# Performance work log

Hardware: AMD Instinct MI355X
Metric: run time of the kernel (lower is better)

## Reference

```python
import jax, jax.numpy as jnp
import numpy as np


def setup_inputs() -> dict:
    key = jax.random.key(0)
    k1, k2 = jax.random.split(key)
    outputs = jax.random.normal(k1, (8192, 64), dtype=jnp.float32)
    labels = jax.random.randint(k2, (8192,), 0, 10)
    return {"outputs": outputs, "labels": labels}


def reference(outputs, labels):
    # outputs: [b, d], labels: [b]
    # Original: distances[i, j] = sqrt(||o_i - o_j||_2) * (-1 if labels differ else 5)
    # for j > i, then summed. sqrt(norm) == (sum of squared diffs) ** 0.25.
    b = outputs.shape[0]
    sq = jnp.sum(outputs * outputs, axis=1)                      # [b]
    gram = outputs @ outputs.T                                   # [b, b]
    d2 = jnp.maximum(sq[:, None] + sq[None, :] - 2.0 * gram, 0.0)  # squared L2 dists
    upper = jnp.triu(jnp.ones((b, b), dtype=bool), k=1)          # j > i mask
    factor = jnp.where(labels[:, None] != labels[None, :], -1.0, 5.0)
    d2_safe = jnp.where(upper, d2, 1.0)                          # avoid 0**0.25 grad issues
    dist = d2_safe ** 0.25                                       # sqrt(L2 norm)
    return jnp.sum(jnp.where(upper, dist * factor, 0.0))
```

## Files before the change

### kernel.cpp

```cpp
#include <hip/hip_runtime.h>


typedef __bf16 bf16x8 __attribute__((ext_vector_type(8)));
typedef float  f32x4  __attribute__((ext_vector_type(4)));
typedef int    i32x4  __attribute__((ext_vector_type(4)));

#define BT    128
#define DK    64
#define PANEL (128 * DK)

__device__ __forceinline__ float qroot(float x) {
    return __builtin_amdgcn_sqrtf(__builtin_amdgcn_sqrtf(x));
}
__device__ __forceinline__ unsigned short rne_bf16(float v) {
    const unsigned u = __builtin_bit_cast(unsigned, v);
    return (unsigned short)((u + 0x7fffu + ((u >> 16) & 1u)) >> 16);
}

__global__ __launch_bounds__(256)
void ss_prep(const float* __restrict__ O, unsigned short* __restrict__ Obf,
             float* __restrict__ sqb) {
    const int row  = blockIdx.x * 4 + (threadIdx.x >> 6);
    const int lane = threadIdx.x & 63;
    const float v = O[(size_t)row * 64 + lane];
    const unsigned short w = rne_bf16(v);
    Obf[(size_t)row * 64 + lane] = w;
    const float wf = __builtin_bit_cast(float, (unsigned)w << 16);
    float s = wf * wf;
    #pragma unroll
    for (int off = 32; off; off >>= 1) s += __shfl_xor(s, off);
    if (lane == 0) sqb[row] = s;
}

__global__ __launch_bounds__(256, 4)
void ss_mfma(const unsigned short* __restrict__ Obf, const float* __restrict__ sqb,
             const int* __restrict__ L, float* __restrict__ partials, int nt) {
    const int t = blockIdx.x;
    const float fnt = (float)nt + 0.5f;
    int ti = (int)floorf(fnt - sqrtf(fnt * fnt - 2.0f * (float)t));
    if (ti < 0) ti = 0;
    if (ti > nt - 1) ti = nt - 1;
    while (ti > 0 && ti * nt - (ti * (ti - 1)) / 2 > t) --ti;
    while ((ti + 1) * nt - ((ti + 1) * ti) / 2 <= t) ++ti;
    const int tj = ti + (t - (ti * nt - (ti * (ti - 1)) / 2));

    const int tid  = threadIdx.x;
    const int wave = tid >> 6, lane = tid & 63;
    const int wr = wave >> 1, wc = wave & 1;
    const bool diag = (ti == tj);

    __shared__ unsigned short lds[2 * PANEL];

    {
        const unsigned short* srcA = Obf + (size_t)(ti * BT) * DK;
        const unsigned short* srcB = Obf + (size_t)(tj * BT) * DK;
        bf16x8 ra[4], rb[4];
        #pragma unroll
        for (int k = 0; k < 4; ++k) {
            const int id = k * 256 + tid;
            ra[k] = *(const bf16x8*)(srcA + id * 8);
            rb[k] = *(const bf16x8*)(srcB + id * 8);
        }
        #pragma unroll
        for (int k = 0; k < 4; ++k) {
            const int id   = k * 256 + tid;
            const int row  = id >> 3, c = id & 7;
            const int slot = (c ^ (row & 7)) * 8;
            *(bf16x8*)(&lds[row * DK + slot])         = ra[k];
            *(bf16x8*)(&lds[PANEL + row * DK + slot]) = rb[k];
        }
    }
    __syncthreads();

    const int lrow = lane & 15;
    const int kq   = lane >> 4;
    const int r0   = ti * BT + wr * 64;
    const int x0   = (kq       ^ (lrow & 7)) * 8;
    const int x1   = ((kq + 4) ^ (lrow & 7)) * 8;

    float accs = 0.0f;

    if (!(diag && (wc < wr))) {
        f32x4 sqi[4]; i32x4 li[4];
        #pragma unroll
        for (int f = 0; f < 4; ++f) {
            const int ib = r0 + f * 16 + (kq << 2);
            sqi[f] = *(const f32x4*)(sqb + ib);
            li[f]  = *(const i32x4*)(L + ib);
        }
        const bool masked = diag && (wr == wc);

        bf16x8 afr[4][2];
        #pragma unroll
        for (int i = 0; i < 4; ++i) {
            const int rbase = (wr * 64 + i * 16 + lrow) * DK;
            afr[i][0] = *(const bf16x8*)(&lds[rbase + x0]);
            afr[i][1] = *(const bf16x8*)(&lds[rbase + x1]);
        }

        #pragma unroll
        for (int jh = 0; jh < 2; ++jh) {
            bf16x8 bfr[2][2];
            #pragma unroll
            for (int g = 0; g < 2; ++g) {
                const int rbase = PANEL + (wc * 64 + jh * 32 + g * 16 + lrow) * DK;
                bfr[g][0] = *(const bf16x8*)(&lds[rbase + x0]);
                bfr[g][1] = *(const bf16x8*)(&lds[rbase + x1]);
            }

            f32x4 acc[4][2];
            #pragma unroll
            for (int i = 0; i < 4; ++i)
                #pragma unroll
                for (int g = 0; g < 2; ++g)
                    acc[i][g] = (f32x4){0.f, 0.f, 0.f, 0.f};

            #pragma unroll
            for (int i = 0; i < 4; ++i)
                #pragma unroll
                for (int g = 0; g < 2; ++g) {
                    acc[i][g] = __builtin_amdgcn_mfma_f32_16x16x32_bf16(afr[i][0], bfr[g][0], acc[i][g], 0, 0, 0);
                    acc[i][g] = __builtin_amdgcn_mfma_f32_16x16x32_bf16(afr[i][1], bfr[g][1], acc[i][g], 0, 0, 0);
                }

            const int c0 = tj * BT + wc * 64 + jh * 32;
            #pragma unroll
            for (int g = 0; g < 2; ++g) {
                const int j    = c0 + g * 16 + lrow;
                const float sj = sqb[j];
                const int  ljv = L[j];
                if (masked) {
                    #pragma unroll
                    for (int fi = 0; fi < 4; ++fi) {
                        const int ib = r0 + fi * 16 + (kq << 2);
                        #pragma unroll
                        for (int r = 0; r < 4; ++r) {
                            float d2 = fmaf(-2.0f, acc[fi][g][r], sqi[fi][r] + sj);
                            d2 = fmaxf(d2, 0.0f);
                            const float dist = qroot(d2);
                            const float fac  = (li[fi][r] != ljv) ? -1.0f : 5.0f;
                            accs += (j > ib + r) ? dist * fac : 0.0f;
                        }
                    }
                } else {
                    #pragma unroll
                    for (int fi = 0; fi < 4; ++fi) {
                        #pragma unroll
                        for (int r = 0; r < 4; ++r) {
                            float d2 = fmaf(-2.0f, acc[fi][g][r], sqi[fi][r] + sj);
                            d2 = fmaxf(d2, 0.0f);
                            const float dist = qroot(d2);
                            const float fac  = (li[fi][r] != ljv) ? -1.0f : 5.0f;
                            accs = fmaf(dist, fac, accs);
                        }
                    }
                }
            }
        }
    }

    #pragma unroll
    for (int off = 32; off > 0; off >>= 1) accs += __shfl_down(accs, off);
    __syncthreads();
    float* fsc = (float*)lds;
    if (lane == 0) fsc[wave] = accs;
    __syncthreads();
    if (tid == 0) partials[t] = (fsc[0] + fsc[1]) + (fsc[2] + fsc[3]);
}

__global__ void ss_reduce_kernel(const float* __restrict__ partials, int n,
                                 float* __restrict__ out) {
    __shared__ float s[4];
    const int tid = threadIdx.x;
    float acc = 0.0f;
    for (int idx = tid; idx < n; idx += 256) acc += partials[idx];
    #pragma unroll
    for (int off = 32; off > 0; off >>= 1) acc += __shfl_down(acc, off);
    if ((tid & 63) == 0) s[tid >> 6] = acc;
    __syncthreads();
    if (tid == 0) out[0] = (s[0] + s[1]) + (s[2] + s[3]);
}

extern "C" void kernel_launch(void* const* d_in, const int* in_sizes, int n_in,
                              void* d_out, int out_size, void* d_ws, size_t ws_size,
                              hipStream_t stream) {
    const float* O = (const float*)d_in[0];
    const int*   L = (const int*)d_in[1];
    float* out = (float*)d_out;

    const int b    = in_sizes[1];
    const int nt   = b / BT;
    const int ntri = nt * (nt + 1) / 2;

    char* ws = (char*)d_ws;
    float*          partials = (float*)ws;
    float*          sqb      = (float*)(ws + (64 << 10));
    unsigned short* Obf      = (unsigned short*)(ws + (128 << 10));

    ss_prep<<<b / 4, 256, 0, stream>>>(O, Obf, sqb);
    ss_mfma<<<ntri, 256, 0, stream>>>(Obf, sqb, L, partials, nt);
    ss_reduce_kernel<<<1, 256, 0, stream>>>(partials, ntri, out);
}
```

Baseline: 30.36 us.

## Switch to per-wave 64x64 triangle tiles with wave-private LDS and no block sync

Each wave now owns one 64x64 upper-triangular tile pair and stages its own A/B panels into a private LDS slice, replacing the 128x128 block tile shared by four waves. Barriers and the LDS cross-wave reduction go away, and diagonal-tile waste drops because sub-tiles below the diagonal are no longer launched idle. The cost is more global loads per output element, since panels are reused across fewer outputs, and more partials to reduce. With nt=128 the triangle count is 8256, which is even, so ntri/2 blocks cover every tile.

```diff
diff --git a/kernel.cpp b/kernel.cpp
--- a/kernel.cpp
+++ b/kernel.cpp
@@ -5,9 +5,9 @@
 typedef float  f32x4  __attribute__((ext_vector_type(4)));
 typedef int    i32x4  __attribute__((ext_vector_type(4)));
 
-#define BT    128
-#define DK    64
-#define PANEL (128 * DK)
+#define WT     64
+#define DK     64
+#define WPANEL (WT * DK)
 
 __device__ __forceinline__ float qroot(float x) {
     return __builtin_amdgcn_sqrtf(__builtin_amdgcn_sqrtf(x));
@@ -32,10 +32,13 @@
     if (lane == 0) sqb[row] = s;
 }
 
-__global__ __launch_bounds__(256, 4)
+__global__ __launch_bounds__(128, 2)
 void ss_mfma(const unsigned short* __restrict__ Obf, const float* __restrict__ sqb,
              const int* __restrict__ L, float* __restrict__ partials, int nt) {
-    const int t = blockIdx.x;
+    const int tid  = threadIdx.x;
+    const int wave = tid >> 6, lane = tid & 63;
+    const int t    = blockIdx.x * 2 + wave;
+
     const float fnt = (float)nt + 0.5f;
     int ti = (int)floorf(fnt - sqrtf(fnt * fnt - 2.0f * (float)t));
     if (ti < 0) ti = 0;
@@ -43,116 +46,111 @@
     while (ti > 0 && ti * nt - (ti * (ti - 1)) / 2 > t) --ti;
     while ((ti + 1) * nt - ((ti + 1) * ti) / 2 <= t) ++ti;
     const int tj = ti + (t - (ti * nt - (ti * (ti - 1)) / 2));
-
-    const int tid  = threadIdx.x;
-    const int wave = tid >> 6, lane = tid & 63;
-    const int wr = wave >> 1, wc = wave & 1;
     const bool diag = (ti == tj);
 
-    __shared__ unsigned short lds[2 * PANEL];
+    const int lrow = lane & 15;
+    const int kq   = lane >> 4;
+    const int r0   = ti * WT;
+
+    __shared__ unsigned short lds[2 * 2 * WPANEL];
+    unsigned short* ldsA = &lds[wave * 2 * WPANEL];
+    unsigned short* ldsB = ldsA + WPANEL;
 
     {
-        const unsigned short* srcA = Obf + (size_t)(ti * BT) * DK;
-        const unsigned short* srcB = Obf + (size_t)(tj * BT) * DK;
-        bf16x8 ra[4], rb[4];
+        const unsigned short* srcA = Obf + (size_t)(ti * WT) * DK;
+        const unsigned short* srcB = Obf + (size_t)(tj * WT) * DK;
+        bf16x8 ra[8], rb[8];
         #pragma unroll
-        for (int k = 0; k < 4; ++k) {
-            const int id = k * 256 + tid;
+        for (int k = 0; k < 8; ++k) {
+            const int id = k * 64 + lane;
             ra[k] = *(const bf16x8*)(srcA + id * 8);
             rb[k] = *(const bf16x8*)(srcB + id * 8);
         }
         #pragma unroll
-        for (int k = 0; k < 4; ++k) {
-            const int id   = k * 256 + tid;
+        for (int k = 0; k < 8; ++k) {
+            const int id   = k * 64 + lane;
             const int row  = id >> 3, c = id & 7;
             const int slot = (c ^ (row & 7)) * 8;
-            *(bf16x8*)(&lds[row * DK + slot])         = ra[k];
-            *(bf16x8*)(&lds[PANEL + row * DK + slot]) = rb[k];
+            *(bf16x8*)(&ldsA[row * DK + slot]) = ra[k];
+            *(bf16x8*)(&ldsB[row * DK + slot]) = rb[k];
         }
     }
-    __syncthreads();
 
-    const int lrow = lane & 15;
-    const int kq   = lane >> 4;
-    const int r0   = ti * BT + wr * 64;
-    const int x0   = (kq       ^ (lrow & 7)) * 8;
-    const int x1   = ((kq + 4) ^ (lrow & 7)) * 8;
+    const int x0 = (kq       ^ (lrow & 7)) * 8;
+    const int x1 = ((kq + 4) ^ (lrow & 7)) * 8;
+
+    f32x4 sqi[4]; i32x4 li[4];
+    #pragma unroll
+    for (int f = 0; f < 4; ++f) {
+        const int ib = r0 + f * 16 + (kq << 2);
+        sqi[f] = *(const f32x4*)(sqb + ib);
+        li[f]  = *(const i32x4*)(L + ib);
+    }
+
+    bf16x8 afr[4][2];
+    #pragma unroll
+    for (int i = 0; i < 4; ++i) {
+        const int rbase = (i * 16 + lrow) * DK;
+        afr[i][0] = *(const bf16x8*)(&ldsA[rbase + x0]);
+        afr[i][1] = *(const bf16x8*)(&ldsA[rbase + x1]);
+    }
 
     float accs = 0.0f;
 
-    if (!(diag && (wc < wr))) {
-        f32x4 sqi[4]; i32x4 li[4];
+    #pragma unroll
+    for (int jh = 0; jh < 2; ++jh) {
+        bf16x8 bfr[2][2];
         #pragma unroll
-        for (int f = 0; f < 4; ++f) {
-            const int ib = r0 + f * 16 + (kq << 2);
-            sqi[f] = *(const f32x4*)(sqb + ib);
-            li[f]  = *(const i32x4*)(L + ib);
-        }
-        const bool masked = diag && (wr == wc);
-
-        bf16x8 afr[4][2];
-        #pragma unroll
-        for (int i = 0; i < 4; ++i) {
-            const int rbase = (wr * 64 + i * 16 + lrow) * DK;
-            afr[i][0] = *(const bf16x8*)(&lds[rbase + x0]);
-            afr[i][1] = *(const bf16x8*)(&lds[rbase + x1]);
+        for (int g = 0; g < 2; ++g) {
+            const int rbase = (jh * 32 + g * 16 + lrow) * DK;
+            bfr[g][0] = *(const bf16x8*)(&ldsB[rbase + x0]);
+            bfr[g][1] = *(const bf16x8*)(&ldsB[rbase + x1]);
         }
 
+        f32x4 acc[4][2];
         #pragma unroll
-        for (int jh = 0; jh < 2; ++jh) {
-            bf16x8 bfr[2][2];
+        for (int i = 0; i < 4; ++i)
+            #pragma unroll
+            for (int g = 0; g < 2; ++g)
+                acc[i][g] = (f32x4){0.f, 0.f, 0.f, 0.f};
+
+        #pragma unroll
+        for (int i = 0; i < 4; ++i)
             #pragma unroll
             for (int g = 0; g < 2; ++g) {
-                const int rbase = PANEL + (wc * 64 + jh * 32 + g * 16 + lrow) * DK;
-                bfr[g][0] = *(const bf16x8*)(&lds[rbase + x0]);
-                bfr[g][1] = *(const bf16x8*)(&lds[rbase + x1]);
+                acc[i][g] = __builtin_amdgcn_mfma_f32_16x16x32_bf16(afr[i][0], bfr[g][0], acc[i][g], 0, 0, 0);
+                acc[i][g] = __builtin_amdgcn_mfma_f32_16x16x32_bf16(afr[i][1], bfr[g][1], acc[i][g], 0, 0, 0);
             }
 
-            f32x4 acc[4][2];
-            #pragma unroll
-            for (int i = 0; i < 4; ++i)
+        const int c0 = tj * WT + jh * 32;
+        #pragma unroll
+        for (int g = 0; g < 2; ++g) {
+            const int j    = c0 + g * 16 + lrow;
+            const float sj = sqb[j];
+            const int  ljv = L[j];
+            if (diag) {
                 #pragma unroll
-                for (int g = 0; g < 2; ++g)
-                    acc[i][g] = (f32x4){0.f, 0.f, 0.f, 0.f};
-
-            #pragma unroll
-            for (int i = 0; i < 4; ++i)
+                for (int fi = 0; fi < 4; ++fi) {
+                    const int ib = r0 + fi * 16 + (kq << 2);
+                    #pragma unroll
+                    for (int r = 0; r < 4; ++r) {
+                        float d2 = fmaf(-2.0f, acc[fi][g][r], sqi[fi][r] + sj);
+                        d2 = fmaxf(d2, 0.0f);
+                        const float dist = qroot(d2);
+                        const float fac  = (li[fi][r] != ljv) ? -1.0f : 5.0f;
+                        accs += (j > ib + r) ? dist * fac : 0.0f;
+                    }
+                }
+            } else {
                 #pragma unroll
-                for (int g = 0; g < 2; ++g) {
-                    acc[i][g] = __builtin_amdgcn_mfma_f32_16x16x32_bf16(afr[i][0], bfr[g][0], acc[i][g], 0, 0, 0);
-                    acc[i][g] = __builtin_amdgcn_mfma_f32_16x16x32_bf16(afr[i][1], bfr[g][1], acc[i][g], 0, 0, 0);
-                }
-
-            const int c0 = tj * BT + wc * 64 + jh * 32;
-            #pragma unroll
-            for (int g = 0; g < 2; ++g) {
-                const int j    = c0 + g * 16 + lrow;
-                const float sj = sqb[j];
-                const int  ljv = L[j];
-                if (masked) {
+                for (int fi = 0; fi < 4; ++fi) {
                     #pragma unroll
-                    for (int fi = 0; fi < 4; ++fi) {
-                        const int ib = r0 + fi * 16 + (kq << 2);
-                        #pragma unroll
-                        for (int r = 0; r < 4; ++r) {
-                            float d2 = fmaf(-2.0f, acc[fi][g][r], sqi[fi][r] + sj);
-                            d2 = fmaxf(d2, 0.0f);
-                            const float dist = qroot(d2);
-                            const float fac  = (li[fi][r] != ljv) ? -1.0f : 5.0f;
-                            accs += (j > ib + r) ? dist * fac : 0.0f;
-                        }
-                    }
-                } else {
-                    #pragma unroll
-                    for (int fi = 0; fi < 4; ++fi) {
-                        #pragma unroll
-                        for (int r = 0; r < 4; ++r) {
-                            float d2 = fmaf(-2.0f, acc[fi][g][r], sqi[fi][r] + sj);
-                            d2 = fmaxf(d2, 0.0f);
-                            const float dist = qroot(d2);
-                            const float fac  = (li[fi][r] != ljv) ? -1.0f : 5.0f;
-                            accs = fmaf(dist, fac, accs);
-                        }
+                    for (int r = 0; r < 4; ++r) {
+                        float d2 = fmaf(-2.0f, acc[fi][g][r], sqi[fi][r] + sj);
+                        d2 = fmaxf(d2, 0.0f);
+                        const float dist = qroot(d2);
+                        const float fac  = (li[fi][r] != ljv) ? -1.0f : 5.0f;
+                        accs = fmaf(dist, fac, accs);
                     }
                 }
             }
@@ -161,11 +159,7 @@
 
     #pragma unroll
     for (int off = 32; off > 0; off >>= 1) accs += __shfl_down(accs, off);
-    __syncthreads();
-    float* fsc = (float*)lds;
-    if (lane == 0) fsc[wave] = accs;
-    __syncthreads();
-    if (tid == 0) partials[t] = (fsc[0] + fsc[1]) + (fsc[2] + fsc[3]);
+    if (lane == 0) partials[t] = accs;
 }
 
 __global__ void ss_reduce_kernel(const float* __restrict__ partials, int n,
@@ -189,7 +183,7 @@
     float* out = (float*)d_out;
 
     const int b    = in_sizes[1];
-    const int nt   = b / BT;
+    const int nt   = b / WT;
     const int ntri = nt * (nt + 1) / 2;
 
     char* ws = (char*)d_ws;
@@ -198,6 +192,6 @@
     unsigned short* Obf      = (unsigned short*)(ws + (128 << 10));
 
     ss_prep<<<b / 4, 256, 0, stream>>>(O, Obf, sqb);
-    ss_mfma<<<ntri, 256, 0, stream>>>(Obf, sqb, L, partials, nt);
+    ss_mfma<<<ntri / 2, 128, 0, stream>>>(Obf, sqb, L, partials, nt);
     ss_reduce_kernel<<<1, 256, 0, stream>>>(partials, ntri, out);
 }
```

New measurement: 38.73 us. +27.6%, slower.
